# Optimization experiments

Measured on AMD Instinct MI355X. Metric: run time of the kernel, lower is better.

The kernel has to match this reference:

```python
import jax, jax.numpy as jnp
import numpy as np

N = 16384      # nodes per graph (128x128 image)
E = 9 * N      # 8-neighborhood + self edges
C = 512        # input feature channels
M = 32         # matrixSize


def _p(key, shape, scale=0.05):
    return jax.random.normal(key, shape, dtype=jnp.float32) * scale


def setup_inputs() -> dict:
    key = jax.random.key(0)
    ks = jax.random.split(key, 40)
    inp = {
        "cF": jax.random.normal(ks[0], (N, C), dtype=jnp.float32),
        "sF": jax.random.normal(ks[1], (N, C), dtype=jnp.float32),
        "content_edge_index": jax.random.randint(ks[2], (2, E), 0, N),
        "content_selections": jax.random.randint(ks[3], (E,), 0, 9),
        "style_edge_index": jax.random.randint(ks[4], (2, E), 0, N),
        "style_selections": jax.random.randint(ks[5], (E,), 0, 9),
        "compress_W": _p(ks[6], (1, C, M)),   # kernel_size=1 -> 1 selection
        "compress_b": _p(ks[7], (M,)),
        "unzip_W": _p(ks[8], (1, M, C)),
        "unzip_b": _p(ks[9], (C,)),
    }
    i = 10
    for net in ("cnet", "snet"):
        for j, (ci, co) in enumerate([(C, 256), (256, 128), (128, M)], 1):
            inp[f"{net}_W{j}"] = _p(ks[i], (9, ci, co)); i += 1  # kernel_size=3 -> 9 selections
            inp[f"{net}_b{j}"] = _p(ks[i], (co,)); i += 1
        inp[f"{net}_fcW"] = _p(ks[i], (M * M, M * M)); i += 1   # torch Linear [out,in]
        inp[f"{net}_fcb"] = _p(ks[i], (M * M,)); i += 1
    return inp


def sel_conv(x, edge_index, sel, W, b):
    """SelectionConv: per-selection weight, gather from src, scatter-add to dst.
    x: [N,Cin], W: [S,Cin,Cout]. Edges with selection >= S are masked (kernel_size=1)."""
    S = W.shape[0]
    t = jnp.einsum('nc,scd->snd', x, W)              # [S, N, Cout]
    src, dst = edge_index[0], edge_index[1]
    msgs = t[jnp.minimum(sel, S - 1), src]           # [E, Cout]
    msgs = jnp.where((sel < S)[:, None], msgs, 0.0)
    return jax.ops.segment_sum(msgs, dst, num_segments=x.shape[0]) + b


def cnn_net(x, ei, sel, W1, b1, W2, b2, W3, b3, fcW, fcb):
    h = jax.nn.relu(sel_conv(x, ei, sel, W1, b1))
    h = jax.nn.relu(sel_conv(h, ei, sel, W2, b2))
    h = sel_conv(h, ei, sel, W3, b3)                 # [N, M]
    g = (h.T @ h) / h.shape[0]                       # [M, M] gram
    return g.reshape(-1) @ fcW.T + fcb               # [M*M]


def reference(cF, sF, content_edge_index, content_selections, style_edge_index,
              style_selections, compress_W, compress_b, unzip_W, unzip_b,
              cnet_W1, cnet_b1, cnet_W2, cnet_b2, cnet_W3, cnet_b3, cnet_fcW, cnet_fcb,
              snet_W1, snet_b1, snet_W2, snet_b2, snet_W3, snet_b3, snet_fcW, snet_fcb):
    cMean = jnp.mean(cF, axis=0, keepdims=True)
    cFc = cF - cMean
    sMean = jnp.mean(sF, axis=0, keepdims=True)
    sFc = sF - sMean
    compress_content = sel_conv(cFc, content_edge_index, content_selections,
                                compress_W, compress_b)          # [N, M]
    m = compress_W.shape[2]
    cMat = cnn_net(cFc, content_edge_index, content_selections,
                   cnet_W1, cnet_b1, cnet_W2, cnet_b2, cnet_W3, cnet_b3,
                   cnet_fcW, cnet_fcb).reshape(m, m)
    sMat = cnn_net(sFc, style_edge_index, style_selections,
                   snet_W1, snet_b1, snet_W2, snet_b2, snet_W3, snet_b3,
                   snet_fcW, snet_fcb).reshape(m, m)
    transmatrix = sMat @ cMat                                    # [M, M]
    transfeature = (transmatrix @ compress_content.T).T          # [N, M]
    out = sel_conv(transfeature, content_edge_index, content_selections,
                   unzip_W, unzip_b) + sMean                     # [N, 512]
    return (out, transmatrix)
```

## Files before the change

kernel.cpp:

```cpp
#include <hip/hip_runtime.h>
#include <hip/hip_bf16.h>
#include <cstddef>
#include <cstdint>

#define NN 16384
#define EE (9*NN)
#define CC 512

typedef __attribute__((ext_vector_type(4))) float f32x4;
typedef __attribute__((ext_vector_type(8))) short bf16x8;

static inline int idiv(int a, int b){ return (a+b-1)/b; }

__device__ __forceinline__ float bf2f(unsigned short u){
    union{unsigned u; float f;} v; v.u = ((unsigned)u) << 16; return v.f;
}
__device__ __forceinline__ unsigned short f2bf(float f){
    union{float f; unsigned u;} v; v.f = f;
    unsigned r = v.u + 0x7fffu + ((v.u >> 16) & 1u);
    return (unsigned short)(r >> 16);
}

__device__ __forceinline__ void gload16(const void* gsrc, void* ldst){
    __builtin_amdgcn_global_load_lds(
        (const __attribute__((address_space(1))) unsigned int*)gsrc,
        (__attribute__((address_space(3))) unsigned int*)ldst,
        16, 0, 0);
}


__global__ void zero_i(int* __restrict__ p, int n){
    int i = blockIdx.x*256 + threadIdx.x; if (i < n) p[i] = 0;
}

__global__ void colsum2(const float* __restrict__ F0, float* __restrict__ cs0,
                        const float* __restrict__ F1, float* __restrict__ cs1){
    const float* F = blockIdx.z ? F1 : F0;
    float* cs = blockIdx.z ? cs1 : cs0;
    const int RPB = NN/256;
    int r0 = blockIdx.x * RPB;
    int c4 = threadIdx.x;
    float4 s = {0.f,0.f,0.f,0.f};
    for (int r = 0; r < RPB; ++r){
        float4 v = ((const float4*)(F + (size_t)(r0+r)*CC))[c4];
        s.x += v.x; s.y += v.y; s.z += v.z; s.w += v.w;
    }
    atomicAdd(&cs[c4*4+0], s.x);
    atomicAdd(&cs[c4*4+1], s.y);
    atomicAdd(&cs[c4*4+2], s.z);
    atomicAdd(&cs[c4*4+3], s.w);
}

__global__ void center2(const float* __restrict__ F0, const float* __restrict__ cs0,
                        ushort4* __restrict__ o0,
                        const float* __restrict__ F1, const float* __restrict__ cs1,
                        ushort4* __restrict__ o1){
    const float* F = blockIdx.z ? F1 : F0;
    const float* cs = blockIdx.z ? cs1 : cs0;
    ushort4* o = blockIdx.z ? o1 : o0;
    int i = blockIdx.x*256 + threadIdx.x;
    float4 v = ((const float4*)F)[i];
    int c = (i << 2) & (CC-1);
    float4 m = *(const float4*)(cs + c);
    ushort4 r;
    r.x = f2bf(v.x - m.x*(1.f/NN));
    r.y = f2bf(v.y - m.y*(1.f/NN));
    r.z = f2bf(v.z - m.z*(1.f/NN));
    r.w = f2bf(v.w - m.w*(1.f/NN));
    o[i] = r;
}

__global__ void wtransz(const float* __restrict__ W0, unsigned short* __restrict__ Wt0,
                        const float* __restrict__ W1, unsigned short* __restrict__ Wt1,
                        int S, int K, int Cout, int Npad, int Kpad){
    const float* W = blockIdx.z ? W1 : W0;
    unsigned short* Wt = blockIdx.z ? Wt1 : Wt0;
    int idx = blockIdx.x*256 + threadIdx.x;
    if (idx >= Npad*Kpad) return;
    int colp = idx / Kpad, k = idx - colp*Kpad;
    int s = colp / Cout, j = colp - s*Cout;
    float v = 0.f;
    if (s < S && k < K) v = W[((size_t)s*K + k)*Cout + j];
    Wt[idx] = f2bf(v);
}

__global__ void wtrans2z(const float* __restrict__ W0, const float* __restrict__ W1,
                         unsigned short* __restrict__ Wt0, unsigned short* __restrict__ Wt1,
                         int K, int Cout){
    __shared__ float tile[32][129];
    int s = blockIdx.z % 9;
    const float* W = (blockIdx.z < 9) ? W0 : W1;
    unsigned short* Wt = (blockIdx.z < 9) ? Wt0 : Wt1;
    int jb = blockIdx.x*128, kb = blockIdx.y*32;
    const float* Ws = W + (size_t)s*K*Cout;
    for (int r = 0; r < 32; ++r)
        tile[r][threadIdx.x] = Ws[(size_t)(kb+r)*Cout + jb + threadIdx.x];
    __syncthreads();
    int kk = threadIdx.x & 31, j0 = threadIdx.x >> 5;
    for (int jj = j0; jj < 128; jj += 4)
        Wt[(size_t)(s*Cout + jb + jj)*K + kb + kk] = f2bf(tile[kk][jj]);
}

__global__ void csr_count3(const int* __restrict__ cDst, const int* __restrict__ sDst,
                           const int* __restrict__ cSel,
                           int* __restrict__ cCnt, int* __restrict__ sCnt, int* __restrict__ cCnt0){
    int e = blockIdx.x*256 + threadIdx.x;
    if (e >= EE) return;
    int z = blockIdx.z;
    if (z == 0)      atomicAdd(&cCnt[cDst[e]], 1);
    else if (z == 1) atomicAdd(&sCnt[sDst[e]], 1);
    else if (cSel[e] == 0) atomicAdd(&cCnt0[cDst[e]], 1);
}
__global__ void csr_scan3(const int* __restrict__ c0, const int* __restrict__ c1,
                          const int* __restrict__ c2,
                          int* __restrict__ r0, int* __restrict__ r1, int* __restrict__ r2){
    const int* cnt = blockIdx.z==0 ? c0 : (blockIdx.z==1 ? c1 : c2);
    int* rowptr    = blockIdx.z==0 ? r0 : (blockIdx.z==1 ? r1 : r2);
    __shared__ int part[1024];
    int t = threadIdx.x;
    int base = t*16, s = 0;
    int local[16];
    #pragma unroll
    for (int i = 0; i < 16; ++i){ local[i] = s; s += cnt[base+i]; }
    part[t] = s; __syncthreads();
    for (int off = 1; off < 1024; off <<= 1){
        int v = (t >= off) ? part[t-off] : 0;
        __syncthreads();
        part[t] += v;
        __syncthreads();
    }
    int pre = (t == 0) ? 0 : part[t-1];
    #pragma unroll
    for (int i = 0; i < 16; ++i) rowptr[base+i] = pre + local[i];
    if (t == 1023) rowptr[NN] = part[1023];
}
__global__ void csr_fill3(const int* __restrict__ cSrc, const int* __restrict__ cDst,
                          const int* __restrict__ cSel,
                          const int* __restrict__ sSrc, const int* __restrict__ sDst,
                          const int* __restrict__ sSel,
                          const int* __restrict__ cRow, const int* __restrict__ sRow,
                          const int* __restrict__ cRow0,
                          int* __restrict__ cCur, int* __restrict__ sCur, int* __restrict__ cCur0,
                          int* __restrict__ cEl, int* __restrict__ sEl, int* __restrict__ cEl0){
    int e = blockIdx.x*256 + threadIdx.x;
    if (e >= EE) return;
    int z = blockIdx.z;
    if (z == 0){
        int d = cDst[e];
        int p = atomicAdd(&cCur[d], 1);
        cEl[cRow[d] + p] = (cSrc[e] << 4) | cSel[e];
    } else if (z == 1){
        int d = sDst[e];
        int p = atomicAdd(&sCur[d], 1);
        sEl[sRow[d] + p] = (sSrc[e] << 4) | sSel[e];
    } else if (cSel[e] == 0){
        int d = cDst[e];
        int p = atomicAdd(&cCur0[d], 1);
        cEl0[cRow0[d] + p] = cSrc[e];
    }
}

template<typename OutT>
__global__ __launch_bounds__(256, 2)
void mfma_gemm(const unsigned short* __restrict__ A0, const unsigned short* __restrict__ Bt0,
               OutT* __restrict__ C0,
               const unsigned short* __restrict__ A1, const unsigned short* __restrict__ Bt1,
               OutT* __restrict__ C1, int K, int N){
    const unsigned short* A  = blockIdx.z ? A1 : A0;
    const unsigned short* Bt = blockIdx.z ? Bt1 : Bt0;
    OutT* C = blockIdx.z ? C1 : C0;
    __shared__ __align__(16) unsigned short As[128*64];
    __shared__ __align__(16) unsigned short Bs[128*64];
    const int tid  = threadIdx.x;
    const int wave = tid >> 6, lane = tid & 63;
    const int row0 = blockIdx.y << 7, col0 = blockIdx.x << 7;
    const int wm = wave >> 1, wn = wave & 1;
    const int fr = lane & 15, fq = lane >> 4;
    f32x4 acc[4][4] = {};
    for (int k0 = 0; k0 < K; k0 += 64){
        __syncthreads();
        #pragma unroll
        for (int i = 0; i < 4; ++i){
            int chb = (wave*4 + i) * 64;
            int ch  = chb + lane;
            int r   = ch >> 3, c8 = ch & 7;
            gload16((const char*)(A  + (size_t)(row0 + r)*K + k0) + c8*16, As + chb*8);
            gload16((const char*)(Bt + (size_t)(col0 + r)*K + k0) + c8*16, Bs + chb*8);
        }
        __syncthreads();
        #pragma unroll
        for (int ks = 0; ks < 2; ++ks){
            bf16x8 av[4], bv[4];
            #pragma unroll
            for (int m = 0; m < 4; ++m)
                av[m] = *(const bf16x8*)(As + ((wm<<6)+(m<<4)+fr)*64 + (ks<<5) + (fq<<3));
            #pragma unroll
            for (int n = 0; n < 4; ++n)
                bv[n] = *(const bf16x8*)(Bs + ((wn<<6)+(n<<4)+fr)*64 + (ks<<5) + (fq<<3));
            #pragma unroll
            for (int m = 0; m < 4; ++m)
                #pragma unroll
                for (int n = 0; n < 4; ++n)
                    acc[m][n] = __builtin_amdgcn_mfma_f32_16x16x32_bf16(bv[n], av[m], acc[m][n], 0, 0, 0);
        }
    }
    #pragma unroll
    for (int m = 0; m < 4; ++m){
        int row = row0 + (wm<<6) + (m<<4) + fr;
        OutT* crow = C + (size_t)row*N + col0 + (wn<<6) + (fq<<2);
        #pragma unroll
        for (int n = 0; n < 4; ++n){
            if constexpr (sizeof(OutT) == 2){
                unsigned lo = f2bf(acc[m][n][0]) | ((unsigned)f2bf(acc[m][n][1]) << 16);
                unsigned hi = f2bf(acc[m][n][2]) | ((unsigned)f2bf(acc[m][n][3]) << 16);
                uint2 pk; pk.x = lo; pk.y = hi;
                *(uint2*)((unsigned short*)crow + (n<<4)) = pk;
            } else {
                float4 pk; pk.x = acc[m][n][0]; pk.y = acc[m][n][1];
                pk.z = acc[m][n][2]; pk.w = acc[m][n][3];
                *(float4*)((float*)crow + (n<<4)) = pk;
            }
        }
    }
}

template<int NT, typename OutT>
__global__ __launch_bounds__(256, 4)
void gemm_db(const unsigned short* __restrict__ A0, const unsigned short* __restrict__ Bt0,
             OutT* __restrict__ C0,
             const unsigned short* __restrict__ A1, const unsigned short* __restrict__ Bt1,
             OutT* __restrict__ C1, int N){
    constexpr int LDK = NT*32;
    const unsigned short* A  = blockIdx.z ? A1 : A0;
    const unsigned short* Bt = blockIdx.z ? Bt1 : Bt0;
    OutT* C = blockIdx.z ? C1 : C0;
    __shared__ __align__(16) unsigned short lds[2][2][4096];
    const int tid = threadIdx.x, w = tid >> 6, l = tid & 63;
    const int wm = w >> 1, wn = w & 1;
    const int fr = l & 15, fq = l >> 4;
    const int nbx = gridDim.x;
    const int nwg = gridDim.x * gridDim.y;
    int blin = blockIdx.y * nbx + blockIdx.x;
    int sw = (blin & 7) * (nwg >> 3) + (blin >> 3);
    const int bx = sw % nbx, by = sw / nbx;
    const int row0 = by << 7, col0 = bx << 7;

    const unsigned short* gA = A + (size_t)row0 * LDK;
    const unsigned short* gB = Bt + (size_t)col0 * LDK;

    auto STG = [&](int buf, int t){
        #pragma unroll
        for (int mtx = 0; mtx < 2; ++mtx){
            const unsigned short* gb = mtx ? gB : gA;
            #pragma unroll
            for (int ld = 0; ld < 2; ++ld){
                int o = (ld*256 + tid) * 16;
                int row = o >> 6;
                int kb = (o & 63) ^ (((o >> 7) & 3) << 4);
                gload16((const char*)(gb + (size_t)row*LDK + t*32) + kb,
                        (char*)&lds[buf][mtx][0] + o);
            }
        }
    };

    f32x4 acc[4][4] = {};
    STG(0, 0);
    __syncthreads();
    for (int t = 0; t < NT; ++t){
        int cur = t & 1;
        if (t + 1 < NT) STG(cur ^ 1, t + 1);
        bf16x8 av[4], bv[4];
        #pragma unroll
        for (int m = 0; m < 4; ++m){
            int r = wm*64 + m*16 + fr;
            int p = (r*64 + fq*16) ^ (((r >> 1) & 3) << 4);
            av[m] = *(const bf16x8*)((const char*)&lds[cur][0][0] + p);
        }
        #pragma unroll
        for (int n = 0; n < 4; ++n){
            int r = wn*64 + n*16 + fr;
            int p = (r*64 + fq*16) ^ (((r >> 1) & 3) << 4);
            bv[n] = *(const bf16x8*)((const char*)&lds[cur][1][0] + p);
        }
        #pragma unroll
        for (int m = 0; m < 4; ++m)
            #pragma unroll
            for (int n = 0; n < 4; ++n)
                acc[m][n] = __builtin_amdgcn_mfma_f32_16x16x32_bf16(bv[n], av[m], acc[m][n], 0, 0, 0);
        __syncthreads();
    }

    #pragma unroll
    for (int m = 0; m < 4; ++m){
        int row = row0 + wm*64 + m*16 + fr;
        OutT* crow = C + (size_t)row*N + col0 + (wn<<6) + (fq<<2);
        #pragma unroll
        for (int n = 0; n < 4; ++n){
            if constexpr (sizeof(OutT) == 2){
                unsigned lo = f2bf(acc[m][n][0]) | ((unsigned)f2bf(acc[m][n][1]) << 16);
                unsigned hi = f2bf(acc[m][n][2]) | ((unsigned)f2bf(acc[m][n][3]) << 16);
                uint2 pk; pk.x = lo; pk.y = hi;
                *(uint2*)((unsigned short*)crow + (n<<4)) = pk;
            } else {
                float4 pk; pk.x = acc[m][n][0]; pk.y = acc[m][n][1];
                pk.z = acc[m][n][2]; pk.w = acc[m][n][3];
                *(float4*)((float*)crow + (n<<4)) = pk;
            }
        }
    }
}

template<typename TO, bool RELU>
__global__ void gather8z(const int* __restrict__ rp0, const int* __restrict__ el0,
                         const unsigned short* __restrict__ t0, const float* __restrict__ b0,
                         TO* __restrict__ o0,
                         const int* __restrict__ rp1, const int* __restrict__ el1,
                         const unsigned short* __restrict__ t1, const float* __restrict__ b1,
                         TO* __restrict__ o1,
                         int tStride, int coutShift){
    const int* rowptr = blockIdx.z ? rp1 : rp0;
    const int* elist  = blockIdx.z ? el1 : el0;
    const unsigned short* t = blockIdx.z ? t1 : t0;
    const float* bias = blockIdx.z ? b1 : b0;
    TO* out = blockIdx.z ? o1 : o0;
    int idx = blockIdx.x*256 + threadIdx.x;
    int chSh = coutShift - 3;
    int d = idx >> chSh;
    int c0 = (idx & ((1 << chSh) - 1)) << 3;
    float acc[8];
    {
        const float4* bb = (const float4*)(bias + c0);
        float4 a = bb[0], b = bb[1];
        acc[0]=a.x; acc[1]=a.y; acc[2]=a.z; acc[3]=a.w;
        acc[4]=b.x; acc[5]=b.y; acc[6]=b.z; acc[7]=b.w;
    }
    int j1 = rowptr[d+1];
    #pragma unroll 2
    for (int j = rowptr[d]; j < j1; ++j){
        int p = elist[j];
        int s = p & 15, sr = p >> 4;
        bf16x8 v = *(const bf16x8*)(t + (size_t)sr*tStride + (s << coutShift) + c0);
        #pragma unroll
        for (int k = 0; k < 8; ++k) acc[k] += bf2f((unsigned short)v[k]);
    }
    if (RELU){
        #pragma unroll
        for (int k = 0; k < 8; ++k) acc[k] = fmaxf(acc[k], 0.f);
    }
    if constexpr (sizeof(TO) == 2){
        union { bf16x8 v; unsigned short u[8]; } r;
        #pragma unroll
        for (int k = 0; k < 8; ++k) r.u[k] = f2bf(acc[k]);
        *(bf16x8*)((unsigned short*)out + ((size_t)d << coutShift) + c0) = r.v;
    } else {
        float4 a = {acc[0],acc[1],acc[2],acc[3]};
        float4 b = {acc[4],acc[5],acc[6],acc[7]};
        float4* op = (float4*)((float*)out + ((size_t)d << coutShift) + c0);
        op[0] = a; op[1] = b;
    }
}

template<bool ADDV>
__global__ void gather4f(const int* __restrict__ rowptr, const int* __restrict__ elist,
                         const float* __restrict__ t,
                         const float* __restrict__ bias, const float* __restrict__ addvec,
                         float* __restrict__ out, int tStride, int coutShift){
    int idx = blockIdx.x*256 + threadIdx.x;
    int chSh = coutShift - 2;
    int d = idx >> chSh;
    int c0 = (idx & ((1 << chSh) - 1)) << 2;
    float4 bb = *(const float4*)(bias + c0);
    float acc0 = bb.x, acc1 = bb.y, acc2 = bb.z, acc3 = bb.w;
    if (ADDV){
        float4 av = *(const float4*)(addvec + c0);
        acc0 += av.x*(1.f/NN); acc1 += av.y*(1.f/NN);
        acc2 += av.z*(1.f/NN); acc3 += av.w*(1.f/NN);
    }
    int j1 = rowptr[d+1];
    #pragma unroll 2
    for (int j = rowptr[d]; j < j1; ++j){
        int sr = elist[j];
        float4 v = *(const float4*)(t + (size_t)sr*tStride + c0);
        acc0 += v.x; acc1 += v.y; acc2 += v.z; acc3 += v.w;
    }
    float4 r = {acc0, acc1, acc2, acc3};
    *(float4*)(out + ((size_t)d << coutShift) + c0) = r;
}

__global__ void gram2(const float* __restrict__ h0, float* __restrict__ g0,
                      const float* __restrict__ h1, float* __restrict__ g1){
    const float* h = blockIdx.z ? h1 : h0;
    float* g = blockIdx.z ? g1 : g0;
    const int RPB = NN/64;
    int r0 = blockIdx.x*RPB;
    int i = threadIdx.x >> 5, j = threadIdx.x & 31;
    float s = 0.f;
    for (int r = 0; r < RPB; ++r){
        const float* row = h + (size_t)(r0+r)*32;
        s += row[i]*row[j];
    }
    atomicAdd(&g[threadIdx.x], s);
}

__global__ void fc2(const float* __restrict__ g0, const float* __restrict__ fcW0,
                    const float* __restrict__ fcb0, float* __restrict__ o0,
                    const float* __restrict__ g1, const float* __restrict__ fcW1,
                    const float* __restrict__ fcb1, float* __restrict__ o1){
    const float* g   = blockIdx.z ? g1 : g0;
    const float* fcW = blockIdx.z ? fcW1 : fcW0;
    const float* fcb = blockIdx.z ? fcb1 : fcb0;
    float* outMat    = blockIdx.z ? o1 : o0;
    int i = blockIdx.x;
    float s = 0.f;
    for (int j = threadIdx.x; j < 1024; j += 256)
        s += g[j] * (1.f/NN) * fcW[(size_t)i*1024 + j];
    __shared__ float red[256];
    red[threadIdx.x] = s; __syncthreads();
    for (int off = 128; off > 0; off >>= 1){
        if (threadIdx.x < off) red[threadIdx.x] += red[threadIdx.x+off];
        __syncthreads();
    }
    if (threadIdx.x == 0) outMat[i] = red[0] + fcb[i];
}

__global__ void mm32tub(const float* __restrict__ sM, const float* __restrict__ cM,
                        const float* __restrict__ Uw, const float* __restrict__ unzB,
                        const float* __restrict__ scs,
                        float* __restrict__ Tout, unsigned short* __restrict__ TUb){
    __shared__ float Ts[1024];
    int t = threadIdx.x;
    for (int e = t; e < 1024; e += 512){
        int i = e >> 5, j = e & 31;
        float s = 0.f;
        #pragma unroll
        for (int k = 0; k < 32; ++k) s += sM[i*32+k]*cM[k*32+j];
        Ts[e] = s;
        Tout[e] = s;
    }
    __syncthreads();
    float u[32];
    #pragma unroll
    for (int i = 0; i < 32; ++i) u[i] = Uw[i*512 + t];
    unsigned short* row = TUb + (size_t)t*64;
    #pragma unroll
    for (int j = 0; j < 32; ++j){
        float s = 0.f;
        #pragma unroll
        for (int i = 0; i < 32; ++i) s += Ts[i*32+j] * u[i];
        row[j] = f2bf(s);
    }
    row[32] = f2bf(unzB[t] + scs[t]*(1.f/NN));
    #pragma unroll
    for (int j = 33; j < 64; ++j) row[j] = 0;
}

__global__ void cvt_ag(const float* __restrict__ agg, ushort4* __restrict__ o){
    int i = blockIdx.x*256 + threadIdx.x;
    int n = i >> 4, k4 = i & 15;
    ushort4 r = {0,0,0,0};
    if (k4 < 8){
        float4 v = *(const float4*)(agg + (size_t)n*32 + (k4<<2));
        r.x = f2bf(v.x); r.y = f2bf(v.y); r.z = f2bf(v.z); r.w = f2bf(v.w);
    } else if (k4 == 8){
        r.x = 0x3F80;
    }
    o[i] = r;
}

extern "C" void kernel_launch(void* const* d_in, const int* in_sizes, int n_in,
                              void* d_out, int out_size, void* d_ws, size_t ws_size,
                              hipStream_t stream){
    const float* cF   = (const float*)d_in[0];
    const float* sF   = (const float*)d_in[1];
    const int*   cEI  = (const int*)d_in[2];
    const int*   cSel = (const int*)d_in[3];
    const int*   sEI  = (const int*)d_in[4];
    const int*   sSel = (const int*)d_in[5];
    const float* compW= (const float*)d_in[6];
    const float* compB= (const float*)d_in[7];
    const float* unzW = (const float*)d_in[8];
    const float* unzB = (const float*)d_in[9];
    const float* cW1=(const float*)d_in[10]; const float* cB1=(const float*)d_in[11];
    const float* cW2=(const float*)d_in[12]; const float* cB2=(const float*)d_in[13];
    const float* cW3=(const float*)d_in[14]; const float* cB3=(const float*)d_in[15];
    const float* cFW=(const float*)d_in[16]; const float* cFB=(const float*)d_in[17];
    const float* sW1=(const float*)d_in[18]; const float* sB1=(const float*)d_in[19];
    const float* sW2=(const float*)d_in[20]; const float* sB2=(const float*)d_in[21];
    const float* sW3=(const float*)d_in[22]; const float* sB3=(const float*)d_in[23];
    const float* sFW=(const float*)d_in[24]; const float* sFB=(const float*)d_in[25];

    float* out  = (float*)d_out;
    float* Tmat = out + (size_t)NN*CC;

    char* w = (char*)d_ws;
    auto alloc = [&](size_t b)->char*{ char* p = w; w += (b + 255) & ~(size_t)255; return p; };
    float* cCol = (float*)alloc(512*4);
    float* sCol = (float*)alloc(512*4);
    float* cg   = (float*)alloc(1024*4);
    float* sg   = (float*)alloc(1024*4);
    float* cMat = (float*)alloc(1024*4);
    float* sMat = (float*)alloc(1024*4);
    float* zpad = (float*)alloc(32*4);
    int* cCnt = (int*)alloc(NN*4);
    int* cCur = (int*)alloc(NN*4);
    int* sCnt = (int*)alloc(NN*4);
    int* sCur = (int*)alloc(NN*4);
    int* cCnt0= (int*)alloc(NN*4);
    int* cCur0= (int*)alloc(NN*4);
    int* cRow = (int*)alloc((NN+1)*4);
    int* sRow = (int*)alloc((NN+1)*4);
    int* cRow0= (int*)alloc((NN+1)*4);
    int* cEl  = (int*)alloc(EE*4);
    int* sEl  = (int*)alloc(EE*4);
    int* cEl0 = (int*)alloc(EE*4);
    float* ccbuf = (float*)alloc((size_t)NN*32*4);
    float* aggb  = (float*)alloc((size_t)NN*32*4);
    unsigned short* aggB = (unsigned short*)alloc((size_t)NN*64*2);
    unsigned short* TUb  = (unsigned short*)alloc((size_t)512*64*2);
    unsigned short* wtC1 = (unsigned short*)alloc((size_t)2304*512*2);
    unsigned short* wtC2 = (unsigned short*)alloc((size_t)1280*256*2);
    unsigned short* wtC3 = (unsigned short*)alloc((size_t)384*128*2);
    unsigned short* wtS1 = (unsigned short*)alloc((size_t)2304*512*2);
    unsigned short* wtS2 = (unsigned short*)alloc((size_t)1280*256*2);
    unsigned short* wtS3 = (unsigned short*)alloc((size_t)384*128*2);
    unsigned short* wtCo = (unsigned short*)alloc((size_t)128*512*2);
    unsigned short* cFcB = (unsigned short*)alloc((size_t)NN*512*2);
    unsigned short* sFcB = (unsigned short*)alloc((size_t)NN*512*2);
    float* h3c = (float*)alloc((size_t)NN*32*4);
    float* h3s = (float*)alloc((size_t)NN*32*4);
    unsigned short* tC = (unsigned short*)alloc((size_t)NN*2304*2);
    unsigned short* tS = (unsigned short*)alloc((size_t)NN*2304*2);
    float* tFc = (float*)tC;
    unsigned short* h1c = cFcB;
    unsigned short* h1s = sFcB;
    unsigned short* h2c = cFcB + (size_t)NN*256;
    unsigned short* h2s = sFcB + (size_t)NN*256;

    const int* cSrc = cEI; const int* cDst = cEI + EE;
    const int* sSrc = sEI; const int* sDst = sEI + EE;

    int zeroInts = (int)(((char*)cCur0 - (char*)d_ws)/4) + NN;
    zero_i<<<idiv(zeroInts,256),256,0,stream>>>((int*)d_ws, zeroInts);

    colsum2<<<dim3(256,1,2),128,0,stream>>>(cF, cCol, sF, sCol);
    center2<<<dim3(NN*CC/1024,1,2),256,0,stream>>>(cF, cCol, (ushort4*)cFcB,
                                                   sF, sCol, (ushort4*)sFcB);

    wtrans2z<<<dim3(2,16,18),128,0,stream>>>(cW1, sW1, wtC1, wtS1, 512, 256);
    wtrans2z<<<dim3(1,8,18),128,0,stream>>>(cW2, sW2, wtC2, wtS2, 256, 128);
    wtransz<<<dim3(idiv(384*128,256),1,2),256,0,stream>>>(cW3, wtC3, sW3, wtS3, 9,128,32, 384,128);
    wtransz<<<dim3(idiv(128*512,256),1,1),256,0,stream>>>(compW, wtCo, compW, wtCo, 1,512,32, 128,512);

    csr_count3<<<dim3(idiv(EE,256),1,3),256,0,stream>>>(cDst, sDst, cSel, cCnt, sCnt, cCnt0);
    csr_scan3<<<dim3(1,1,3),1024,0,stream>>>(cCnt, sCnt, cCnt0, cRow, sRow, cRow0);
    csr_fill3<<<dim3(idiv(EE,256),1,3),256,0,stream>>>(cSrc,cDst,cSel, sSrc,sDst,sSel,
                                                       cRow,sRow,cRow0, cCur,sCur,cCur0,
                                                       cEl,sEl,cEl0);

    mfma_gemm<float><<<dim3(1,128,1),256,0,stream>>>(cFcB, wtCo, tFc,
                                                     cFcB, wtCo, tFc, 512, 128);
    gather4f<false><<<NN*8/256,256,0,stream>>>(cRow0,cEl0,tFc,compB,nullptr,ccbuf,128,5);

    gather4f<false><<<NN*8/256,256,0,stream>>>(cRow0,cEl0,ccbuf,zpad,nullptr,aggb,32,5);
    cvt_ag<<<NN*16/256,256,0,stream>>>(aggb, (ushort4*)aggB);

    gemm_db<16,unsigned short><<<dim3(18,128,2),256,0,stream>>>(cFcB, wtC1, tC,
                                                                sFcB, wtS1, tS, 2304);
    gather8z<unsigned short,true><<<dim3(2048,1,2),256,0,stream>>>(
        cRow,cEl,tC,cB1,h1c, sRow,sEl,tS,sB1,h1s, 2304, 8);
    gemm_db<8,unsigned short><<<dim3(10,128,2),256,0,stream>>>(h1c, wtC2, tC,
                                                               h1s, wtS2, tS, 1280);
    gather8z<unsigned short,true><<<dim3(1024,1,2),256,0,stream>>>(
        cRow,cEl,tC,cB2,h2c, sRow,sEl,tS,sB2,h2s, 1280, 7);
    mfma_gemm<unsigned short><<<dim3(3,128,2),256,0,stream>>>(h2c, wtC3, tC,
                                                              h2s, wtS3, tS, 128, 384);
    gather8z<float,false><<<dim3(256,1,2),256,0,stream>>>(
        cRow,cEl,tC,cB3,h3c, sRow,sEl,tS,sB3,h3s, 384, 5);
    gram2<<<dim3(64,1,2),1024,0,stream>>>(h3c, cg, h3s, sg);
    fc2<<<dim3(1024,1,2),256,0,stream>>>(cg,cFW,cFB,cMat, sg,sFW,sFB,sMat);

    mm32tub<<<1,512,0,stream>>>(sMat, cMat, unzW, unzB, sCol, Tmat, TUb);
    mfma_gemm<float><<<dim3(4,128,1),256,0,stream>>>(aggB, TUb, out,
                                                     aggB, TUb, out, 64, 512);
}
```

Baseline: 408.2 us.

## Fold mean-centering into GEMM epilogue via precomputed mean·W correction

Instead of writing mean-centered bf16 features in a separate pass, the column-sum kernel now also converts the raw features to bf16 in the same read. The centering is applied algebraically: a small kernel computes mean·W per output column, and the GEMM epilogues subtract it. This removes one full read of both fp32 feature matrices and a kernel launch. It adds a small extra kernel and a per-column load in the epilogues. Precision may drop slightly because uncentered bf16 values are used before the subtraction.

Result: slower. 431.0 us (+5.6%).

```diff
diff --git a/kernel.cpp b/kernel.cpp
--- a/kernel.cpp
+++ b/kernel.cpp
@@ -33,10 +33,13 @@
     int i = blockIdx.x*256 + threadIdx.x; if (i < n) p[i] = 0;
 }
 
-__global__ void colsum2(const float* __restrict__ F0, float* __restrict__ cs0,
-                        const float* __restrict__ F1, float* __restrict__ cs1){
+__global__ void colsum_cvt(const float* __restrict__ F0, float* __restrict__ cs0,
+                           ushort4* __restrict__ o0,
+                           const float* __restrict__ F1, float* __restrict__ cs1,
+                           ushort4* __restrict__ o1){
     const float* F = blockIdx.z ? F1 : F0;
     float* cs = blockIdx.z ? cs1 : cs0;
+    ushort4* o = blockIdx.z ? o1 : o0;
     const int RPB = NN/256;
     int r0 = blockIdx.x * RPB;
     int c4 = threadIdx.x;
@@ -44,6 +47,9 @@
     for (int r = 0; r < RPB; ++r){
         float4 v = ((const float4*)(F + (size_t)(r0+r)*CC))[c4];
         s.x += v.x; s.y += v.y; s.z += v.z; s.w += v.w;
+        ushort4 u;
+        u.x = f2bf(v.x); u.y = f2bf(v.y); u.z = f2bf(v.z); u.w = f2bf(v.w);
+        o[(size_t)(r0+r)*(CC/4) + c4] = u;
     }
     atomicAdd(&cs[c4*4+0], s.x);
     atomicAdd(&cs[c4*4+1], s.y);
@@ -51,23 +57,21 @@
     atomicAdd(&cs[c4*4+3], s.w);
 }
 
-__global__ void center2(const float* __restrict__ F0, const float* __restrict__ cs0,
-                        ushort4* __restrict__ o0,
-                        const float* __restrict__ F1, const float* __restrict__ cs1,
-                        ushort4* __restrict__ o1){
-    const float* F = blockIdx.z ? F1 : F0;
+__global__ void mw_k2(const float* __restrict__ W0, const float* __restrict__ cs0,
+                      float* __restrict__ mw0,
+                      const float* __restrict__ W1, const float* __restrict__ cs1,
+                      float* __restrict__ mw1,
+                      int K, int Cout){
+    const float* W = blockIdx.z ? W1 : W0;
     const float* cs = blockIdx.z ? cs1 : cs0;
-    ushort4* o = blockIdx.z ? o1 : o0;
-    int i = blockIdx.x*256 + threadIdx.x;
-    float4 v = ((const float4*)F)[i];
-    int c = (i << 2) & (CC-1);
-    float4 m = *(const float4*)(cs + c);
-    ushort4 r;
-    r.x = f2bf(v.x - m.x*(1.f/NN));
-    r.y = f2bf(v.y - m.y*(1.f/NN));
-    r.z = f2bf(v.z - m.z*(1.f/NN));
-    r.w = f2bf(v.w - m.w*(1.f/NN));
-    o[i] = r;
+    float* mw = blockIdx.z ? mw1 : mw0;
+    int s = blockIdx.x, j = threadIdx.x;
+    int kpb = K / gridDim.y;
+    int k0 = blockIdx.y * kpb;
+    const float* Wp = W + ((size_t)s*K + k0)*Cout + j;
+    float acc = 0.f;
+    for (int k = 0; k < kpb; ++k) acc += cs[k0+k] * Wp[(size_t)k*Cout];
+    atomicAdd(&mw[s*Cout + j], acc * (1.f/NN));
 }
 
 __global__ void wtransz(const float* __restrict__ W0, unsigned short* __restrict__ Wt0,
@@ -163,12 +167,13 @@
 template<typename OutT>
 __global__ __launch_bounds__(256, 2)
 void mfma_gemm(const unsigned short* __restrict__ A0, const unsigned short* __restrict__ Bt0,
-               OutT* __restrict__ C0,
+               OutT* __restrict__ C0, const float* __restrict__ csub0,
                const unsigned short* __restrict__ A1, const unsigned short* __restrict__ Bt1,
-               OutT* __restrict__ C1, int K, int N){
+               OutT* __restrict__ C1, const float* __restrict__ csub1, int K, int N){
     const unsigned short* A  = blockIdx.z ? A1 : A0;
     const unsigned short* Bt = blockIdx.z ? Bt1 : Bt0;
     OutT* C = blockIdx.z ? C1 : C0;
+    const float* csub = blockIdx.z ? csub1 : csub0;
     __shared__ __align__(16) unsigned short As[128*64];
     __shared__ __align__(16) unsigned short Bs[128*64];
     const int tid  = threadIdx.x;
@@ -210,14 +215,18 @@
         OutT* crow = C + (size_t)row*N + col0 + (wn<<6) + (fq<<2);
         #pragma unroll
         for (int n = 0; n < 4; ++n){
+            float v0 = acc[m][n][0], v1 = acc[m][n][1], v2 = acc[m][n][2], v3 = acc[m][n][3];
+            if (csub){
+                float4 sub = *(const float4*)(csub + col0 + (wn<<6) + (fq<<2) + (n<<4));
+                v0 -= sub.x; v1 -= sub.y; v2 -= sub.z; v3 -= sub.w;
+            }
             if constexpr (sizeof(OutT) == 2){
-                unsigned lo = f2bf(acc[m][n][0]) | ((unsigned)f2bf(acc[m][n][1]) << 16);
-                unsigned hi = f2bf(acc[m][n][2]) | ((unsigned)f2bf(acc[m][n][3]) << 16);
+                unsigned lo = f2bf(v0) | ((unsigned)f2bf(v1) << 16);
+                unsigned hi = f2bf(v2) | ((unsigned)f2bf(v3) << 16);
                 uint2 pk; pk.x = lo; pk.y = hi;
                 *(uint2*)((unsigned short*)crow + (n<<4)) = pk;
             } else {
-                float4 pk; pk.x = acc[m][n][0]; pk.y = acc[m][n][1];
-                pk.z = acc[m][n][2]; pk.w = acc[m][n][3];
+                float4 pk; pk.x = v0; pk.y = v1; pk.z = v2; pk.w = v3;
                 *(float4*)((float*)crow + (n<<4)) = pk;
             }
         }
@@ -227,13 +236,14 @@
 template<int NT, typename OutT>
 __global__ __launch_bounds__(256, 4)
 void gemm_db(const unsigned short* __restrict__ A0, const unsigned short* __restrict__ Bt0,
-             OutT* __restrict__ C0,
+             OutT* __restrict__ C0, const float* __restrict__ csub0,
              const unsigned short* __restrict__ A1, const unsigned short* __restrict__ Bt1,
-             OutT* __restrict__ C1, int N){
+             OutT* __restrict__ C1, const float* __restrict__ csub1, int N){
     constexpr int LDK = NT*32;
     const unsigned short* A  = blockIdx.z ? A1 : A0;
     const unsigned short* Bt = blockIdx.z ? Bt1 : Bt0;
     OutT* C = blockIdx.z ? C1 : C0;
+    const float* csub = blockIdx.z ? csub1 : csub0;
     __shared__ __align__(16) unsigned short lds[2][2][4096];
     const int tid = threadIdx.x, w = tid >> 6, l = tid & 63;
     const int wm = w >> 1, wn = w & 1;
@@ -296,14 +306,18 @@
         OutT* crow = C + (size_t)row*N + col0 + (wn<<6) + (fq<<2);
         #pragma unroll
         for (int n = 0; n < 4; ++n){
+            float v0 = acc[m][n][0], v1 = acc[m][n][1], v2 = acc[m][n][2], v3 = acc[m][n][3];
+            if (csub){
+                float4 sub = *(const float4*)(csub + col0 + (wn<<6) + (fq<<2) + (n<<4));
+                v0 -= sub.x; v1 -= sub.y; v2 -= sub.z; v3 -= sub.w;
+            }
             if constexpr (sizeof(OutT) == 2){
-                unsigned lo = f2bf(acc[m][n][0]) | ((unsigned)f2bf(acc[m][n][1]) << 16);
-                unsigned hi = f2bf(acc[m][n][2]) | ((unsigned)f2bf(acc[m][n][3]) << 16);
+                unsigned lo = f2bf(v0) | ((unsigned)f2bf(v1) << 16);
+                unsigned hi = f2bf(v2) | ((unsigned)f2bf(v3) << 16);
                 uint2 pk; pk.x = lo; pk.y = hi;
                 *(uint2*)((unsigned short*)crow + (n<<4)) = pk;
             } else {
-                float4 pk; pk.x = acc[m][n][0]; pk.y = acc[m][n][1];
-                pk.z = acc[m][n][2]; pk.w = acc[m][n][3];
+                float4 pk; pk.x = v0; pk.y = v1; pk.z = v2; pk.w = v3;
                 *(float4*)((float*)crow + (n<<4)) = pk;
             }
         }
@@ -501,6 +515,9 @@
     float* cMat = (float*)alloc(1024*4);
     float* sMat = (float*)alloc(1024*4);
     float* zpad = (float*)alloc(32*4);
+    float* mwC1 = (float*)alloc(2304*4);
+    float* mwS1 = (float*)alloc(2304*4);
+    float* mwCo = (float*)alloc(128*4);
     int* cCnt = (int*)alloc(NN*4);
     int* cCur = (int*)alloc(NN*4);
     int* sCnt = (int*)alloc(NN*4);
@@ -542,14 +559,16 @@
     int zeroInts = (int)(((char*)cCur0 - (char*)d_ws)/4) + NN;
     zero_i<<<idiv(zeroInts,256),256,0,stream>>>((int*)d_ws, zeroInts);
 
-    colsum2<<<dim3(256,1,2),128,0,stream>>>(cF, cCol, sF, sCol);
-    center2<<<dim3(NN*CC/1024,1,2),256,0,stream>>>(cF, cCol, (ushort4*)cFcB,
-                                                   sF, sCol, (ushort4*)sFcB);
+    colsum_cvt<<<dim3(256,1,2),128,0,stream>>>(cF, cCol, (ushort4*)cFcB,
+                                               sF, sCol, (ushort4*)sFcB);
 
     wtrans2z<<<dim3(2,16,18),128,0,stream>>>(cW1, sW1, wtC1, wtS1, 512, 256);
     wtrans2z<<<dim3(1,8,18),128,0,stream>>>(cW2, sW2, wtC2, wtS2, 256, 128);
     wtransz<<<dim3(idiv(384*128,256),1,2),256,0,stream>>>(cW3, wtC3, sW3, wtS3, 9,128,32, 384,128);
     wtransz<<<dim3(idiv(128*512,256),1,1),256,0,stream>>>(compW, wtCo, compW, wtCo, 1,512,32, 128,512);
+
+    mw_k2<<<dim3(9,8,2),256,0,stream>>>(cW1, cCol, mwC1, sW1, sCol, mwS1, 512, 256);
+    mw_k2<<<dim3(1,16,1),32,0,stream>>>(compW, cCol, mwCo, compW, cCol, mwCo, 512, 32);
 
     csr_count3<<<dim3(idiv(EE,256),1,3),256,0,stream>>>(cDst, sDst, cSel, cCnt, sCnt, cCnt0);
     csr_scan3<<<dim3(1,1,3),1024,0,stream>>>(cCnt, sCnt, cCnt0, cRow, sRow, cRow0);
@@ -557,29 +576,29 @@
                                                        cRow,sRow,cRow0, cCur,sCur,cCur0,
                                                        cEl,sEl,cEl0);
 
-    mfma_gemm<float><<<dim3(1,128,1),256,0,stream>>>(cFcB, wtCo, tFc,
-                                                     cFcB, wtCo, tFc, 512, 128);
+    mfma_gemm<float><<<dim3(1,128,1),256,0,stream>>>(cFcB, wtCo, tFc, mwCo,
+                                                     cFcB, wtCo, tFc, mwCo, 512, 128);
     gather4f<false><<<NN*8/256,256,0,stream>>>(cRow0,cEl0,tFc,compB,nullptr,ccbuf,128,5);
 
     gather4f<false><<<NN*8/256,256,0,stream>>>(cRow0,cEl0,ccbuf,zpad,nullptr,aggb,32,5);
     cvt_ag<<<NN*16/256,256,0,stream>>>(aggb, (ushort4*)aggB);
 
-    gemm_db<16,unsigned short><<<dim3(18,128,2),256,0,stream>>>(cFcB, wtC1, tC,
-                                                                sFcB, wtS1, tS, 2304);
+    gemm_db<16,unsigned short><<<dim3(18,128,2),256,0,stream>>>(cFcB, wtC1, tC, mwC1,
+                                                                sFcB, wtS1, tS, mwS1, 2304);
     gather8z<unsigned short,true><<<dim3(2048,1,2),256,0,stream>>>(
         cRow,cEl,tC,cB1,h1c, sRow,sEl,tS,sB1,h1s, 2304, 8);
-    gemm_db<8,unsigned short><<<dim3(10,128,2),256,0,stream>>>(h1c, wtC2, tC,
-                                                               h1s, wtS2, tS, 1280);
+    gemm_db<8,unsigned short><<<dim3(10,128,2),256,0,stream>>>(h1c, wtC2, tC, nullptr,
+                                                               h1s, wtS2, tS, nullptr, 1280);
     gather8z<unsigned short,true><<<dim3(1024,1,2),256,0,stream>>>(
         cRow,cEl,tC,cB2,h2c, sRow,sEl,tS,sB2,h2s, 1280, 7);
-    mfma_gemm<unsigned short><<<dim3(3,128,2),256,0,stream>>>(h2c, wtC3, tC,
-                                                              h2s, wtS3, tS, 128, 384);
+    mfma_gemm<unsigned short><<<dim3(3,128,2),256,0,stream>>>(h2c, wtC3, tC, nullptr,
+                                                              h2s, wtS3, tS, nullptr, 128, 384);
     gather8z<float,false><<<dim3(256,1,2),256,0,stream>>>(
         cRow,cEl,tC,cB3,h3c, sRow,sEl,tS,sB3,h3s, 384, 5);
     gram2<<<dim3(64,1,2),1024,0,stream>>>(h3c, cg, h3s, sg);
     fc2<<<dim3(1024,1,2),256,0,stream>>>(cg,cFW,cFB,cMat, sg,sFW,sFB,sMat);
 
     mm32tub<<<1,512,0,stream>>>(sMat, cMat, unzW, unzB, sCol, Tmat, TUb);
-    mfma_gemm<float><<<dim3(4,128,1),256,0,stream>>>(aggB, TUb, out,
-                                                     aggB, TUb, out, 64, 512);
-}
+    mfma_gemm<float><<<dim3(4,128,1),256,0,stream>>>(aggB, TUb, out, nullptr,
+                                                     aggB, TUb, out, nullptr, 64, 512);
+}
```
